# Kernel tuning notes

Hardware: AMD Instinct MI355X
Metric: run time of the kernel (lower is better)

The kernel has to match this reference:

```python
import jax, jax.numpy as jnp
import numpy as np

HIDDEN = 1024
N_HEAD = 16
HEAD_DIM = HIDDEN // N_HEAD  # 64
BATCH = 1
SEQ = 4096
THETA = 10000.0


def _rope_cos_sin(seq_len, head_dim, dtype=jnp.float32):
    # freqs[t, j] = t / theta^(2j/dim), j in [0, dim/2)
    inv_freq = 1.0 / (THETA ** (jnp.arange(0, head_dim, 2, dtype=dtype) / head_dim))
    t = jnp.arange(seq_len, dtype=dtype)
    freqs = jnp.outer(t, inv_freq)           # [S, D/2]
    return jnp.cos(freqs), jnp.sin(freqs)


def _apply_rope(x, cos, sin):
    # x: [B, S, H, D]; pairs (x[...,2j], x[...,2j+1]) rotated by angle freqs[t, j]
    x2 = x.reshape(*x.shape[:-1], -1, 2)       # [B, S, H, D/2, 2]
    x_re, x_im = x2[..., 0], x2[..., 1]
    c = cos[None, :, None, :]                   # [1, S, 1, D/2]
    s = sin[None, :, None, :]
    out_re = x_re * c - x_im * s
    out_im = x_re * s + x_im * c
    out = jnp.stack([out_re, out_im], axis=-1)  # [B, S, H, D/2, 2]
    return out.reshape(x.shape)


def setup_inputs() -> dict:
    key = jax.random.key(0)
    kx, kq, kk, kv = jax.random.split(key, 4)
    scale = 1.0 / np.sqrt(HIDDEN)
    return {
        "x": jax.random.normal(kx, (BATCH, SEQ, HIDDEN), dtype=jnp.float32),
        "wq": jax.random.normal(kq, (HIDDEN, HIDDEN), dtype=jnp.float32) * scale,
        "wk": jax.random.normal(kk, (HIDDEN, HIDDEN), dtype=jnp.float32) * scale,
        "wv": jax.random.normal(kv, (HIDDEN, HIDDEN), dtype=jnp.float32) * scale,
    }


def reference(x, wq, wk, wv):
    B, S, _ = x.shape
    # torch nn.Linear(no bias): y = x @ W.T
    xq = (x @ wq.T).reshape(B, S, N_HEAD, HEAD_DIM).astype(jnp.float32)
    xk = (x @ wk.T).reshape(B, S, N_HEAD, HEAD_DIM).astype(jnp.float32)
    xv = (x @ wv.T).reshape(B, S, N_HEAD, HEAD_DIM).astype(jnp.float32)

    cos, sin = _rope_cos_sin(S, HEAD_DIM)
    q = _apply_rope(xq, cos, sin)
    k = _apply_rope(xk, cos, sin)

    # [B, H, S, S] scores, no causal mask (matches source)
    scores = jnp.einsum("bqhd,bkhd->bhqk", q, k) / jnp.sqrt(
        jnp.asarray(HEAD_DIM, dtype=q.dtype))
    attn = jax.nn.softmax(scores, axis=-1)
    out = jnp.einsum("bhqk,bkhd->bqhd", attn, xv)  # [B, S, H, D]
    return out.reshape(B, S, N_HEAD * HEAD_DIM)
```

## Files before the change

### kernel.cpp

```cpp
#include <hip/hip_runtime.h>
#include <stdint.h>


#define SEQLEN 4096
#define NHEAD 16
#define HDIM 64

typedef __bf16 bf16x8 __attribute__((ext_vector_type(8)));
typedef float f32x4 __attribute__((ext_vector_type(4)));
typedef float f32x16 __attribute__((ext_vector_type(16)));

__device__ __forceinline__ unsigned short f2bf(float f) {
  union { float f; unsigned int u; } v; v.f = f;
  unsigned int r = v.u + 0x7FFFu + ((v.u >> 16) & 1u);
  return (unsigned short)(r >> 16);
}
__device__ __forceinline__ unsigned int pkc(float lo, float hi) {
  union { __bf16 b[2]; unsigned int u; } z;
  z.b[0] = (__bf16)lo; z.b[1] = (__bf16)hi;
  return z.u;
}
__device__ __forceinline__ bf16x8 as_bf(uint4 v) { return __builtin_bit_cast(bf16x8, v); }
__device__ __forceinline__ f32x4 mfma16(bf16x8 a, bf16x8 b, f32x4 c) {
  return __builtin_amdgcn_mfma_f32_16x16x32_bf16(a, b, c, 0, 0, 0);
}
__device__ __forceinline__ f32x16 mfma32(bf16x8 a, bf16x8 b, f32x16 c) {
  return __builtin_amdgcn_mfma_f32_32x32x16_bf16(a, b, c, 0, 0, 0);
}

__global__ __launch_bounds__(256) void k_convert(
    const float* __restrict__ x, const float* __restrict__ wq,
    const float* __restrict__ wk, const float* __restrict__ wv,
    unsigned short* __restrict__ xbf, unsigned short* __restrict__ wbf) {
  int i = blockIdx.x * 256 + threadIdx.x;
  const int NX = SEQLEN * 1024 / 4;
  const int NW = 1024 * 1024 / 4;
  float4 v;
  unsigned short* dst;
  int di;
  if (i < NX) {
    v = ((const float4*)x)[i]; dst = xbf; di = i;
  } else {
    int j = i - NX;
    const float4* src = (const float4*)((j < NW) ? wq : (j < 2 * NW) ? wk : wv);
    v = src[j & (NW - 1)];
    dst = wbf; di = j;
  }
  ushort4 o; o.x = f2bf(v.x); o.y = f2bf(v.y); o.z = f2bf(v.z); o.w = f2bf(v.w);
  ((ushort4*)dst)[di] = o;
}

__global__ __launch_bounds__(256) void k_table(float* __restrict__ ct, float* __restrict__ st) {
  int i = blockIdx.x * 256 + threadIdx.x;
  int s = i >> 5, j = i & 31;
  double inv = exp(-(double)j * 0.28782313662425572);
  double a = (double)s * inv;
  ct[i] = (float)cos(a);
  st[i] = (float)sin(a);
}

__global__ __launch_bounds__(256) void k_gemm(
    const unsigned short* __restrict__ xbf, const unsigned short* __restrict__ wbf,
    const float* __restrict__ ct, const float* __restrict__ st,
    unsigned short* __restrict__ qbf, unsigned short* __restrict__ kbf,
    unsigned short* __restrict__ vT) {
  __shared__ __align__(16) unsigned short As[2][128 * 40];
  __shared__ __align__(16) unsigned short Bs[2][128 * 40];
  const int t = threadIdx.x;
  const int bn = blockIdx.x, bm = blockIdx.y;
  const int lane = t & 63, wave = t >> 6;
  const int r = lane & 15, g = lane >> 4;
  const int wm = wave >> 1, wn = wave & 1;

  const int c0 = t, c1 = t + 256;
  const int ar0 = c0 >> 2, ao0 = (c0 & 3) * 16;
  const int ar1 = c1 >> 2, ao1 = (c1 & 3) * 16;
  const char* Ab = (const char*)xbf;
  const char* Bb = (const char*)wbf;

  uint4 ra0, ra1, rb0, rb1;
#define LD_TILE(kk)                                                             \
  ra0 = *(const uint4*)(Ab + (size_t)(bm * 128 + ar0) * 2048 + (kk) * 64 + ao0); \
  ra1 = *(const uint4*)(Ab + (size_t)(bm * 128 + ar1) * 2048 + (kk) * 64 + ao1); \
  rb0 = *(const uint4*)(Bb + (size_t)(bn * 128 + ar0) * 2048 + (kk) * 64 + ao0); \
  rb1 = *(const uint4*)(Bb + (size_t)(bn * 128 + ar1) * 2048 + (kk) * 64 + ao1);

  LD_TILE(0)
  f32x4 zero4 = {0.f, 0.f, 0.f, 0.f};
  f32x4 acc[4][4];
#pragma unroll
  for (int m = 0; m < 4; ++m)
#pragma unroll
    for (int n = 0; n < 4; ++n) acc[m][n] = zero4;

  for (int kk = 0; kk < 32; ++kk) {
    unsigned short* Ac = As[kk & 1];
    unsigned short* Bc = Bs[kk & 1];
    *(uint4*)((char*)Ac + ar0 * 80 + ao0) = ra0;
    *(uint4*)((char*)Ac + ar1 * 80 + ao1) = ra1;
    *(uint4*)((char*)Bc + ar0 * 80 + ao0) = rb0;
    *(uint4*)((char*)Bc + ar1 * 80 + ao1) = rb1;
    __syncthreads();
    if (kk < 31) { LD_TILE(kk + 1) }
    bf16x8 af[4], bfr[4];
#pragma unroll
    for (int m = 0; m < 4; ++m)
      af[m] = as_bf(*(const uint4*)((const char*)Ac + (wm * 64 + m * 16 + r) * 80 + g * 16));
#pragma unroll
    for (int n = 0; n < 4; ++n)
      bfr[n] = as_bf(*(const uint4*)((const char*)Bc + (wn * 64 + n * 16 + r) * 80 + g * 16));
#pragma unroll
    for (int m = 0; m < 4; ++m)
#pragma unroll
      for (int n = 0; n < 4; ++n)
        acc[m][n] = mfma16(af[m], bfr[n], acc[m][n]);
  }

  const int matid = bn >> 3;
#pragma unroll
  for (int m = 0; m < 4; ++m) {
    const int row0 = bm * 128 + wm * 64 + m * 16 + 4 * g;
#pragma unroll
    for (int n = 0; n < 4; ++n) {
      const int col = bn * 128 + wn * 64 + n * 16 + r;
      const int d = col & 63;
      const int hh = (col >> 6) & 15;
      if (matid < 2) {
        const int jdx = (col >> 1) & 31;
        const float sgn = (col & 1) ? 1.0f : -1.0f;
        unsigned short* dst = (matid == 0) ? qbf : kbf;
        const float qs = (matid == 0) ? 0.18033688011112042f : 1.0f;
#pragma unroll
        for (int j = 0; j < 4; ++j) {
          float v = acc[m][n][j];
          float p = __shfl_xor(v, 1);
          int srow = row0 + j;
          float cv = ct[srow * 32 + jdx];
          float sv = st[srow * 32 + jdx];
          float o = (v * cv + p * sv * sgn) * qs;
          dst[(size_t)srow * 1024 + (hh * 64 + d)] = f2bf(o);
        }
      } else {
        ushort4 o;
        o.x = f2bf(acc[m][n][0]); o.y = f2bf(acc[m][n][1]);
        o.z = f2bf(acc[m][n][2]); o.w = f2bf(acc[m][n][3]);
        *(ushort4*)&vT[((size_t)(hh * 64 + d)) * SEQLEN + row0] = o;
      }
    }
  }
}

__global__ __launch_bounds__(512) void k_attn(
    const unsigned short* __restrict__ qbf, const unsigned short* __restrict__ kbf,
    const unsigned short* __restrict__ vT, float* __restrict__ out) {
  __shared__ __align__(16) char smem[65536];
  const int t = threadIdx.x;
  const int b = blockIdx.x;
  const int work = (b & 7) * 64 + (b >> 3);
  const int h = work >> 5;
  const int qb = work & 31;
  const int lane = t & 63, wave = t >> 6;
  const int qw = wave & 3, hf = wave >> 2;
  const int li = lane & 31, hi = lane >> 5;
  const int q0 = qb * 128 + qw * 32;

  bf16x8 qf[4];
#pragma unroll
  for (int c = 0; c < 4; ++c)
    qf[c] = as_bf(*(const uint4*)((const char*)qbf +
              (size_t)(q0 + li) * 2048 + h * 128 + c * 32 + hi * 16));

  f32x16 z16 = {0.f};
  f32x16 acc[2];
  acc[0] = z16; acc[1] = z16;
  float mrun = -1e30f, lrun = 0.f;

  const int tt = t & 255;
  const int srow = tt >> 2, sbyte = (tt & 3) * 16;
  const int swz = (srow & 7) << 4;
  const int wa0 = srow * 128 + (sbyte ^ swz);
  const int wa1 = srow * 128 + ((sbyte + 64) ^ swz);
  const char* kg = (const char*)kbf + h * 128;
  const char* vg = (const char*)vT + (size_t)h * HDIM * SEQLEN * 2;
  char* base = smem + hf * 32768;

  uint4 rk0, rk1, rv0, rv1;
#define LD_KV64(kt)                                                            \
  rk0 = *(const uint4*)(kg + (size_t)((kt) * 64 + srow) * 2048 + sbyte);       \
  rk1 = *(const uint4*)(kg + (size_t)((kt) * 64 + srow) * 2048 + sbyte + 64);  \
  rv0 = *(const uint4*)(vg + (size_t)srow * 8192 + (kt) * 128 + sbyte);        \
  rv1 = *(const uint4*)(vg + (size_t)srow * 8192 + (kt) * 128 + sbyte + 64);

  LD_KV64(hf * 32)

  const int frsw = (lane & 7) << 4;

  for (int j = 0; j < 32; ++j) {
    char* Kb = base + (j & 1) * 8192;
    char* Vb = base + 16384 + (j & 1) * 8192;
    *(uint4*)(Kb + wa0) = rk0;
    *(uint4*)(Kb + wa1) = rk1;
    *(uint4*)(Vb + wa0) = rv0;
    *(uint4*)(Vb + wa1) = rv1;
    __syncthreads();
    if (j < 31) { LD_KV64(hf * 32 + j + 1) }

    f32x16 sT[2];
    sT[0] = z16; sT[1] = z16;
    __builtin_amdgcn_s_setprio(1);
#pragma unroll
    for (int c = 0; c < 4; ++c) {
      const int co = (((2 * c + hi) * 16) ^ frsw);
      bf16x8 k0 = as_bf(*(const uint4*)(Kb + li * 128 + co));
      bf16x8 k1 = as_bf(*(const uint4*)(Kb + (32 + li) * 128 + co));
      sT[0] = mfma32(k0, qf[c], sT[0]);
      sT[1] = mfma32(k1, qf[c], sT[1]);
    }
    __builtin_amdgcn_s_setprio(0);

    float tm[16];
#pragma unroll
    for (int i = 0; i < 16; ++i) tm[i] = fmaxf(sT[0][i], sT[1][i]);
#pragma unroll
    for (int sft = 8; sft >= 1; sft >>= 1)
#pragma unroll
      for (int i = 0; i < 8; ++i)
        if (i < sft) tm[i] = fmaxf(tm[i], tm[i + sft]);
    float tmax = fmaxf(tm[0], __shfl_xor(tm[0], 32));

    if (!__all(tmax <= mrun + 8.0f)) {
      float mnew = fmaxf(mrun, tmax);
      float alpha = __builtin_amdgcn_exp2f(mrun - mnew);
      mrun = mnew;
      lrun *= alpha;
#pragma unroll
      for (int dt = 0; dt < 2; ++dt)
#pragma unroll
        for (int i = 0; i < 16; ++i) acc[dt][i] *= alpha;
    }
#pragma unroll
    for (int s = 0; s < 2; ++s)
#pragma unroll
      for (int i = 0; i < 16; ++i) sT[s][i] = __builtin_amdgcn_exp2f(sT[s][i] - mrun);
    float sum8[8];
#pragma unroll
    for (int i = 0; i < 8; ++i) sum8[i] = (sT[0][i] + sT[0][i + 8]) + (sT[1][i] + sT[1][i + 8]);
#pragma unroll
    for (int sft = 4; sft >= 1; sft >>= 1)
#pragma unroll
      for (int i = 0; i < 4; ++i)
        if (i < sft) sum8[i] += sum8[i + sft];
    lrun += sum8[0];

#pragma unroll
    for (int kc = 0; kc < 4; ++kc) {
      const int sub = kc >> 1, bix = (kc & 1) * 8;
      unsigned U0 = pkc(sT[sub][bix + 0], sT[sub][bix + 1]);
      unsigned U1 = pkc(sT[sub][bix + 2], sT[sub][bix + 3]);
      unsigned U2 = pkc(sT[sub][bix + 4], sT[sub][bix + 5]);
      unsigned U3 = pkc(sT[sub][bix + 6], sT[sub][bix + 7]);
      unsigned X0 = (unsigned)__shfl_xor((int)U0, 32);
      unsigned X1 = (unsigned)__shfl_xor((int)U1, 32);
      unsigned X2 = (unsigned)__shfl_xor((int)U2, 32);
      unsigned X3 = (unsigned)__shfl_xor((int)U3, 32);
      uint4 bw;
      bw.x = hi ? X2 : U0;
      bw.y = hi ? X3 : U1;
      bw.z = hi ? U2 : X0;
      bw.w = hi ? U3 : X1;
      bf16x8 pfr = as_bf(bw);
      const int vo = (((2 * kc + hi) * 16) ^ frsw);
      __builtin_amdgcn_s_setprio(1);
#pragma unroll
      for (int dt = 0; dt < 2; ++dt) {
        bf16x8 vf = as_bf(*(const uint4*)(Vb + (32 * dt + li) * 128 + vo));
        acc[dt] = mfma32(vf, pfr, acc[dt]);
      }
      __builtin_amdgcn_s_setprio(0);
    }
  }

  float lhalf = lrun + __shfl_xor(lrun, 32);

  __syncthreads();
  float* shm = (float*)smem;
  if (hf == 1) {
    float* ab = shm + qw * 2048;
#pragma unroll
    for (int dt = 0; dt < 2; ++dt)
#pragma unroll
      for (int i = 0; i < 16; ++i) {
        int d = (i & 3) + 8 * (i >> 2) + 4 * hi + 32 * dt;
        ab[d * 32 + li] = acc[dt][i];
      }
    if (hi == 0) {
      shm[8192 + qw * 64 + li] = mrun;
      shm[8192 + qw * 64 + 32 + li] = lhalf;
    }
  }
  __syncthreads();
  if (hf == 0) {
    float* ab = shm + qw * 2048;
    float m1 = shm[8192 + qw * 64 + li];
    float l1 = shm[8192 + qw * 64 + 32 + li];
    float mf = fmaxf(mrun, m1);
    float a0 = __builtin_amdgcn_exp2f(mrun - mf);
    float a1 = __builtin_amdgcn_exp2f(m1 - mf);
    float linv = 1.0f / (a0 * lhalf + a1 * l1);
#pragma unroll
    for (int dt = 0; dt < 2; ++dt)
#pragma unroll
      for (int i = 0; i < 16; ++i) {
        int d = (i & 3) + 8 * (i >> 2) + 4 * hi + 32 * dt;
        acc[dt][i] = (a0 * acc[dt][i] + a1 * ab[d * 32 + li]) * linv;
      }
    __asm__ volatile("" ::: "memory");

    float* eb = shm + qw * 2048;
#pragma unroll
    for (int dt = 0; dt < 2; ++dt) {
#pragma unroll
      for (int i = 0; i < 16; ++i)
        eb[li * 33 + ((i & 3) + 8 * (i >> 2) + 4 * hi)] = acc[dt][i];
      __asm__ volatile("" ::: "memory");
#pragma unroll
      for (int it = 0; it < 16; ++it) {
        int q = it * 2 + hi;
        float v = eb[q * 33 + li];
        out[(size_t)(q0 + q) * 1024 + h * 64 + dt * 32 + li] = v;
      }
      __asm__ volatile("" ::: "memory");
    }
  }
}

extern "C" void kernel_launch(void* const* d_in, const int* in_sizes, int n_in,
                              void* d_out, int out_size, void* d_ws, size_t ws_size,
                              hipStream_t stream) {
  const float* x  = (const float*)d_in[0];
  const float* wq = (const float*)d_in[1];
  const float* wk = (const float*)d_in[2];
  const float* wv = (const float*)d_in[3];
  float* out = (float*)d_out;
  char* ws = (char*)d_ws;

  unsigned short* qbf = (unsigned short*)(ws);
  unsigned short* kbf = (unsigned short*)(ws + ((size_t)8 << 20));
  unsigned short* vT  = (unsigned short*)(ws + ((size_t)16 << 20));
  unsigned short* xbf = (unsigned short*)(ws + ((size_t)24 << 20));
  unsigned short* wbf = (unsigned short*)(ws + ((size_t)32 << 20));
  float* ct = (float*)(ws + ((size_t)38 << 20));
  float* st = (float*)(ws + ((size_t)38 << 20) + ((size_t)512 << 10));

  k_convert<<<dim3(7168), dim3(256), 0, stream>>>(x, wq, wk, wv, xbf, wbf);
  k_table<<<dim3(512), dim3(256), 0, stream>>>(ct, st);
  k_gemm<<<dim3(24, 32), dim3(256), 0, stream>>>(xbf, wbf, ct, st, qbf, kbf, vT);
  k_attn<<<dim3(512), dim3(512), 0, stream>>>(qbf, kbf, vT, out);
}
```

Baseline: 180.5 us.

## Load K/V fragments directly from global into registers, dropping LDS staging

Removes the double-buffered LDS staging of K and V tiles and the per-iteration __syncthreads. Each wave now loads its MFMA operand fragments straight from global memory, relying on L1/L2 for reuse. Shared memory shrinks to only the final cross-wave reduction buffer, and launch bounds request more resident waves per SIMD. In exchange, the four query waves each fetch the same K/V data redundantly, and global load latency is no longer prefetched one iteration ahead.

```diff
diff --git a/kernel.cpp b/kernel.cpp
--- a/kernel.cpp
+++ b/kernel.cpp
@@ -150,10 +150,10 @@
   }
 }
 
-__global__ __launch_bounds__(512) void k_attn(
+__global__ __launch_bounds__(512, 4) void k_attn(
     const unsigned short* __restrict__ qbf, const unsigned short* __restrict__ kbf,
     const unsigned short* __restrict__ vT, float* __restrict__ out) {
-  __shared__ __align__(16) char smem[65536];
+  __shared__ float shm[8448];
   const int t = threadIdx.x;
   const int b = blockIdx.x;
   const int work = (b & 7) * 64 + (b >> 3);
@@ -175,48 +175,33 @@
   acc[0] = z16; acc[1] = z16;
   float mrun = -1e30f, lrun = 0.f;
 
-  const int tt = t & 255;
-  const int srow = tt >> 2, sbyte = (tt & 3) * 16;
-  const int swz = (srow & 7) << 4;
-  const int wa0 = srow * 128 + (sbyte ^ swz);
-  const int wa1 = srow * 128 + ((sbyte + 64) ^ swz);
-  const char* kg = (const char*)kbf + h * 128;
-  const char* vg = (const char*)vT + (size_t)h * HDIM * SEQLEN * 2;
-  char* base = smem + hf * 32768;
-
-  uint4 rk0, rk1, rv0, rv1;
-#define LD_KV64(kt)                                                            \
-  rk0 = *(const uint4*)(kg + (size_t)((kt) * 64 + srow) * 2048 + sbyte);       \
-  rk1 = *(const uint4*)(kg + (size_t)((kt) * 64 + srow) * 2048 + sbyte + 64);  \
-  rv0 = *(const uint4*)(vg + (size_t)srow * 8192 + (kt) * 128 + sbyte);        \
-  rv1 = *(const uint4*)(vg + (size_t)srow * 8192 + (kt) * 128 + sbyte + 64);
-
-  LD_KV64(hf * 32)
-
-  const int frsw = (lane & 7) << 4;
+  const char* pK0 = (const char*)kbf + (size_t)(hf * 32 * 64 + li) * 2048 + h * 128 + hi * 16;
+  const char* pK1 = pK0 + 32 * 2048;
+  const char* pV  = (const char*)vT + ((size_t)h * 64 + li) * 8192 + hf * 32 * 128 + hi * 16;
 
   for (int j = 0; j < 32; ++j) {
-    char* Kb = base + (j & 1) * 8192;
-    char* Vb = base + 16384 + (j & 1) * 8192;
-    *(uint4*)(Kb + wa0) = rk0;
-    *(uint4*)(Kb + wa1) = rk1;
-    *(uint4*)(Vb + wa0) = rv0;
-    *(uint4*)(Vb + wa1) = rv1;
-    __syncthreads();
-    if (j < 31) { LD_KV64(hf * 32 + j + 1) }
-
+    bf16x8 k0[4], k1[4];
+#pragma unroll
+    for (int c = 0; c < 4; ++c) {
+      k0[c] = as_bf(*(const uint4*)(pK0 + c * 32));
+      k1[c] = as_bf(*(const uint4*)(pK1 + c * 32));
+    }
     f32x16 sT[2];
     sT[0] = z16; sT[1] = z16;
     __builtin_amdgcn_s_setprio(1);
 #pragma unroll
     for (int c = 0; c < 4; ++c) {
-      const int co = (((2 * c + hi) * 16) ^ frsw);
-      bf16x8 k0 = as_bf(*(const uint4*)(Kb + li * 128 + co));
-      bf16x8 k1 = as_bf(*(const uint4*)(Kb + (32 + li) * 128 + co));
-      sT[0] = mfma32(k0, qf[c], sT[0]);
-      sT[1] = mfma32(k1, qf[c], sT[1]);
+      sT[0] = mfma32(k0[c], qf[c], sT[0]);
+      sT[1] = mfma32(k1[c], qf[c], sT[1]);
     }
     __builtin_amdgcn_s_setprio(0);
+
+    bf16x8 vf[2][4];
+#pragma unroll
+    for (int dt = 0; dt < 2; ++dt)
+#pragma unroll
+      for (int kc = 0; kc < 4; ++kc)
+        vf[dt][kc] = as_bf(*(const uint4*)(pV + (size_t)dt * 32 * 8192 + kc * 32));
 
     float tm[16];
 #pragma unroll
@@ -269,21 +254,17 @@
       bw.z = hi ? U2 : X0;
       bw.w = hi ? U3 : X1;
       bf16x8 pfr = as_bf(bw);
-      const int vo = (((2 * kc + hi) * 16) ^ frsw);
       __builtin_amdgcn_s_setprio(1);
-#pragma unroll
-      for (int dt = 0; dt < 2; ++dt) {
-        bf16x8 vf = as_bf(*(const uint4*)(Vb + (32 * dt + li) * 128 + vo));
-        acc[dt] = mfma32(vf, pfr, acc[dt]);
-      }
+      acc[0] = mfma32(vf[0][kc], pfr, acc[0]);
+      acc[1] = mfma32(vf[1][kc], pfr, acc[1]);
       __builtin_amdgcn_s_setprio(0);
     }
+    pK0 += 64 * 2048; pK1 += 64 * 2048; pV += 128;
   }
 
   float lhalf = lrun + __shfl_xor(lrun, 32);
 
   __syncthreads();
-  float* shm = (float*)smem;
   if (hf == 1) {
     float* ab = shm + qw * 2048;
 #pragma unroll
```

Result: slower. 310.7 us (+72.1%).

## Permute V fragment loads to match P layout, removing cross-lane shuffles

Applied to the files above, without the earlier changes.

Instead of exchanging packed P values between lane halves with shfl_xor before each PV MFMA, the V operand is now loaded with a permuted k ordering (two 8-byte reads per fragment) that matches the P register layout directly. V fragments for all k-chunks are also hoisted ahead of the softmax so LDS latency can overlap with the max/exp math. The row-max reduction is reshaped to start from 8 partial values. The cost is twice as many, narrower LDS reads and more live registers for the preloaded V fragments.

```diff
diff --git a/kernel.cpp b/kernel.cpp
--- a/kernel.cpp
+++ b/kernel.cpp
@@ -218,13 +218,27 @@
     }
     __builtin_amdgcn_s_setprio(0);
 
-    float tm[16];
-#pragma unroll
-    for (int i = 0; i < 16; ++i) tm[i] = fmaxf(sT[0][i], sT[1][i]);
-#pragma unroll
-    for (int sft = 8; sft >= 1; sft >>= 1)
-#pragma unroll
-      for (int i = 0; i < 8; ++i)
+    bf16x8 vf[2][4];
+#pragma unroll
+    for (int dt = 0; dt < 2; ++dt) {
+      const int vrow = (dt * 32 + li) * 128;
+#pragma unroll
+      for (int kc = 0; kc < 4; ++kc) {
+        uint2 vlo = *(const uint2*)(Vb + vrow + (((kc * 32) ^ frsw) + hi * 8));
+        uint2 vhi = *(const uint2*)(Vb + vrow + (((kc * 32 + 16) ^ frsw) + hi * 8));
+        uint4 vv; vv.x = vlo.x; vv.y = vlo.y; vv.z = vhi.x; vv.w = vhi.y;
+        vf[dt][kc] = as_bf(vv);
+      }
+    }
+
+    float tm[8];
+#pragma unroll
+    for (int i = 0; i < 8; ++i)
+      tm[i] = fmaxf(fmaxf(sT[0][i], sT[0][i + 8]), fmaxf(sT[1][i], sT[1][i + 8]));
+#pragma unroll
+    for (int sft = 4; sft >= 1; sft >>= 1)
+#pragma unroll
+      for (int i = 0; i < 4; ++i)
         if (i < sft) tm[i] = fmaxf(tm[i], tm[i + sft]);
     float tmax = fmaxf(tm[0], __shfl_xor(tm[0], 32));
 
@@ -255,27 +269,15 @@
 #pragma unroll
     for (int kc = 0; kc < 4; ++kc) {
       const int sub = kc >> 1, bix = (kc & 1) * 8;
-      unsigned U0 = pkc(sT[sub][bix + 0], sT[sub][bix + 1]);
-      unsigned U1 = pkc(sT[sub][bix + 2], sT[sub][bix + 3]);
-      unsigned U2 = pkc(sT[sub][bix + 4], sT[sub][bix + 5]);
-      unsigned U3 = pkc(sT[sub][bix + 6], sT[sub][bix + 7]);
-      unsigned X0 = (unsigned)__shfl_xor((int)U0, 32);
-      unsigned X1 = (unsigned)__shfl_xor((int)U1, 32);
-      unsigned X2 = (unsigned)__shfl_xor((int)U2, 32);
-      unsigned X3 = (unsigned)__shfl_xor((int)U3, 32);
       uint4 bw;
-      bw.x = hi ? X2 : U0;
-      bw.y = hi ? X3 : U1;
-      bw.z = hi ? U2 : X0;
-      bw.w = hi ? U3 : X1;
+      bw.x = pkc(sT[sub][bix + 0], sT[sub][bix + 1]);
+      bw.y = pkc(sT[sub][bix + 2], sT[sub][bix + 3]);
+      bw.z = pkc(sT[sub][bix + 4], sT[sub][bix + 5]);
+      bw.w = pkc(sT[sub][bix + 6], sT[sub][bix + 7]);
       bf16x8 pfr = as_bf(bw);
-      const int vo = (((2 * kc + hi) * 16) ^ frsw);
       __builtin_amdgcn_s_setprio(1);
-#pragma unroll
-      for (int dt = 0; dt < 2; ++dt) {
-        bf16x8 vf = as_bf(*(const uint4*)(Vb + (32 * dt + li) * 128 + vo));
-        acc[dt] = mfma32(vf, pfr, acc[dt]);
-      }
+      acc[0] = mfma32(vf[0][kc], pfr, acc[0]);
+      acc[1] = mfma32(vf[1][kc], pfr, acc[1]);
       __builtin_amdgcn_s_setprio(0);
     }
   }
```

After: 168.3 us. -6.8%, faster.
